# Kernel optimization log

Measured on AMD Instinct MI355X. Metric: run time of the kernel, lower is better.

## Reference

```python
import jax, jax.numpy as jnp
import numpy as np

TEMP = 0.07
POS_WINDOW = 2
EPS = 1e-8
NEG = -1e9  # finite large-negative for masking (safe under vjp)


def _l2norm(x):
    # matches F.normalize(dim=-1) with eps=1e-12
    n = jnp.sqrt(jnp.sum(x * x, axis=-1, keepdims=True))
    return x / jnp.maximum(n, 1e-12)


def setup_inputs() -> dict:
    key = jax.random.key(0)
    k1, k2, k3, k4, k5 = jax.random.split(key, 5)
    B, T, D = 32, 1024, 256
    eeg_enc = jax.random.normal(k1, (B, T, D), dtype=jnp.float32)
    eye_enc = jax.random.normal(k2, (B, T, D), dtype=jnp.float32)
    mask = jax.random.randint(k3, (B, T), 0, 2, dtype=jnp.int32)
    W_eeg = jax.random.normal(k4, (D, D), dtype=jnp.float32) / np.sqrt(D)
    W_eye = jax.random.normal(k5, (D, D), dtype=jnp.float32) / np.sqrt(D)
    return {"eeg_enc": eeg_enc, "eye_enc": eye_enc, "mask": mask,
            "W_eeg": W_eeg, "W_eye": W_eye}


def reference(eeg_enc, eye_enc, mask, W_eeg, W_eye):
    B, T, D = eeg_enc.shape
    valid = mask > 0  # (B,T)
    # nn.Linear(bias=False): x @ W.T, then L2-normalize
    e = _l2norm(jnp.einsum('btd,ed->bte', eeg_enc, W_eeg))
    v = _l2norm(jnp.einsum('btd,ed->bte', eye_enc, W_eye))
    sims = jnp.einsum('bid,bjd->bij', e, v) / TEMP  # (B,T,T)
    # rank of each valid step within the compressed (gathered) ordering
    rank = jnp.cumsum(valid.astype(jnp.int32), axis=-1) - 1  # (B,T)
    band = jnp.abs(rank[:, :, None] - rank[:, None, :]) <= POS_WINDOW
    pair = valid[:, :, None] & valid[:, None, :]  # both steps valid
    pos = pair & band
    # per-row max over positive (banded) entries
    pos_scores = jnp.max(jnp.where(pos, sims, NEG), axis=-1)  # (B,T)
    # logsumexp over valid columns (the gathered sims row)
    lse = jax.nn.logsumexp(jnp.where(valid[:, None, :], sims, NEG), axis=-1)
    row_loss = -(pos_scores - lse)  # (B,T)
    Tv = jnp.sum(valid, axis=-1)  # (B,)
    per_b = jnp.sum(jnp.where(valid, row_loss, 0.0), axis=-1) / jnp.maximum(Tv, 1)
    per_b = jnp.where(Tv >= 2, per_b, 0.0)  # skip samples with <2 valid steps
    return jnp.sum(per_b) / (B + EPS)
```

## Files before the change

### kernel.cpp

```cpp
#include <hip/hip_runtime.h>
#include <hip/hip_bf16.h>

typedef __attribute__((ext_vector_type(8))) short bf16x8;
typedef __attribute__((ext_vector_type(4))) float f32x4;

#define INVT (1.0f/0.07f)

static __device__ __forceinline__ short f2bf(float f){
    unsigned int u = __float_as_uint(f);
    unsigned int r = (u + 0x7fffu + ((u >> 16) & 1u)) >> 16;
    return (short)r;
}
static __device__ __forceinline__ float bf2f(short s){
    return __uint_as_float(((unsigned int)(unsigned short)s) << 16);
}

static __device__ __forceinline__ void gld16(const void* g, void* l){
    __builtin_amdgcn_global_load_lds(
        (const __attribute__((address_space(1))) unsigned int*)g,
        (__attribute__((address_space(3))) unsigned int*)l, 16, 0, 0);
}

__global__ __launch_bounds__(256) void prep_kernel(const float* __restrict__ Weeg,
                                                   const float* __restrict__ Weye,
                                                   const int* __restrict__ mask,
                                                   short* __restrict__ Wout,
                                                   int* __restrict__ rank,
                                                   int* __restrict__ idx,
                                                   int* __restrict__ Tv,
                                                   float* __restrict__ cb,
                                                   float* __restrict__ bsum){
    __shared__ int ssum[256];
    int tid = threadIdx.x;
    if (blockIdx.x < 512){
        int i = blockIdx.x * 256 + tid;
        float v = (i < 65536) ? Weeg[i] : Weye[i - 65536];
        Wout[i] = f2bf(v);
        return;
    }
    int b = blockIdx.x - 512;
    if (tid == 0) bsum[b] = 0.f;
    int local[4]; int s = 0;
    #pragma unroll
    for (int q = 0; q < 4; ++q){
        int t = tid*4 + q;
        local[q] = (mask[b*1024 + t] > 0) ? 1 : 0;
        s += local[q];
    }
    ssum[tid] = s;
    __syncthreads();
    for (int off = 1; off < 256; off <<= 1){
        int add = (tid >= off) ? ssum[tid - off] : 0;
        __syncthreads();
        ssum[tid] += add;
        __syncthreads();
    }
    int run = ssum[tid] - s;
    #pragma unroll
    for (int q = 0; q < 4; ++q){
        int t = tid*4 + q;
        int g = b*1024 + t;
        run += local[q];
        rank[g] = run - 1;
        cb[g]   = local[q] ? 0.0f : -1e9f;
        if (local[q]) idx[b*1024 + run - 1] = t;
    }
    if (tid == 255) Tv[b] = ssum[255];
}

__global__ __launch_bounds__(256, 5) void proj_kernel(const float* __restrict__ Aeeg,
                                                      const float* __restrict__ Aeye,
                                                      const short* __restrict__ Wbf,
                                                      short* __restrict__ Eout,
                                                      short* __restrict__ Vout){
    __shared__ short sW[64 * 256];
    int sel = blockIdx.y;
    const float* A   = sel ? Aeye : Aeeg;
    const short* W   = Wbf + sel * 65536;
    short*       Out = sel ? Vout : Eout;

    int tid = threadIdx.x;
    int w = tid >> 6, lane = tid & 63;
    int l15 = lane & 15, lq = lane >> 4;
    int kb  = lq * 8;
    int row0 = blockIdx.x * 64;

    bf16x8 xf[8];
    {
        const float* ap = A + (size_t)(row0 + w*16 + l15) * 256 + kb;
        #pragma unroll
        for (int g = 0; g < 8; ++g){
            float4 x0 = *(const float4*)(ap + g*32);
            float4 x1 = *(const float4*)(ap + g*32 + 4);
            bf16x8 t;
            t[0]=f2bf(x0.x); t[1]=f2bf(x0.y); t[2]=f2bf(x0.z); t[3]=f2bf(x0.w);
            t[4]=f2bf(x1.x); t[5]=f2bf(x1.y); t[6]=f2bf(x1.z); t[7]=f2bf(x1.w);
            xf[g] = t;
        }
    }

    f32x4 acc[16];
    #pragma unroll
    for (int q = 0; q < 16; ++q) acc[q] = (f32x4){0.f,0.f,0.f,0.f};

    int ro   = lane >> 5;
    int cb_s = lane & 31;
    int s7   = l15 & 7;

    #pragma unroll
    for (int pass = 0; pass < 4; ++pass){
        if (pass) __syncthreads();
        #pragma unroll
        for (int p = 0; p < 8; ++p){
            int rl  = w*16 + p*2 + ro;
            int cbg = cb_s ^ ((p*2 + ro) & 7);
            gld16(W + (size_t)(pass*64 + rl)*256 + cbg*8,
                  &sW[(w*16 + p*2) * 256]);
        }
        __syncthreads();
        #pragma unroll
        for (int nt = 0; nt < 4; ++nt){
            f32x4 c = acc[pass*4 + nt];
            int rbase = (nt*16 + l15) * 256;
            #pragma unroll
            for (int g = 0; g < 8; ++g){
                bf16x8 wf = *(const bf16x8*)&sW[rbase + (((g*4 + lq) ^ s7) << 3)];
                c = __builtin_amdgcn_mfma_f32_16x16x32_bf16(wf, xf[g], c, 0, 0, 0);
            }
            acc[pass*4 + nt] = c;
        }
    }

    float ss = 0.f;
    #pragma unroll
    for (int q = 0; q < 16; ++q){
        #pragma unroll
        for (int r = 0; r < 4; ++r){ float x = acc[q][r]; ss += x*x; }
    }
    ss += __shfl_xor(ss, 16);
    ss += __shfl_xor(ss, 32);
    float scale = 1.0f / fmaxf(sqrtf(ss), 1e-12f);

    short* op = Out + (size_t)(row0 + w*16 + l15) * 256 + lq*4;
    #pragma unroll
    for (int q = 0; q < 16; ++q){
        short4 pk;
        pk.x = f2bf(acc[q][0] * scale);
        pk.y = f2bf(acc[q][1] * scale);
        pk.z = f2bf(acc[q][2] * scale);
        pk.w = f2bf(acc[q][3] * scale);
        *(short4*)(op + ((q >> 2) * 64 + (q & 3) * 16)) = pk;
    }
}

__global__ __launch_bounds__(256, 2) void loss_kernel(const short* __restrict__ E,
                                                      const short* __restrict__ V,
                                                      const float* __restrict__ cb,
                                                      float* __restrict__ psum){
    __shared__ short sV[2][64 * 256];
    __shared__ float sRed[4][32];

    int n  = blockIdx.x;
    int m  = n >> 3;
    int b  = ((m >> 6) << 3) | (n & 7);
    int lm = m & 63;
    int i0 = (lm >> 3) * 128;
    int jb = lm & 7;
    int j0 = jb * 128;

    int tid = threadIdx.x;
    int w = tid >> 6, lane = tid & 63;
    int l15 = lane & 15, lq = lane >> 4;
    int kb = lq * 8;
    int s7 = l15 & 7;

    int ro = lane >> 5;
    int cs = lane & 31;
    const short* Vrow = V + ((size_t)b*1024 + j0 + w*16 + ro) * 256;
    #pragma unroll
    for (int p = 0; p < 8; ++p){
        int rr = (p*2 + ro) & 7;
        gld16(Vrow + (size_t)(p*2)*256 + (size_t)((cs ^ rr) * 8),
              &sV[0][(w*16 + p*2) * 256]);
    }

    bf16x8 af[2][8];
    {
        const short* ep = E + ((size_t)b*1024 + i0 + w*32 + l15) * 256 + kb;
        #pragma unroll
        for (int g = 0; g < 8; ++g){
            af[0][g] = *(const bf16x8*)(ep + g*32);
            af[1][g] = *(const bf16x8*)(ep + 16*256 + g*32);
        }
    }

    float cbv[8];
    #pragma unroll
    for (int ct = 0; ct < 8; ++ct)
        cbv[ct] = cb[b*1024 + j0 + ct*16 + l15];

    f32x4 acc[2][8];
    #pragma unroll
    for (int s = 0; s < 2; ++s)
        #pragma unroll
        for (int ct = 0; ct < 8; ++ct) acc[s][ct] = (f32x4){0.f,0.f,0.f,0.f};

    __syncthreads();

    #pragma unroll
    for (int p = 0; p < 8; ++p){
        int rr = (p*2 + ro) & 7;
        gld16(Vrow + (size_t)(64 + p*2)*256 + (size_t)((cs ^ rr) * 8),
              &sV[1][(w*16 + p*2) * 256]);
    }

    #pragma unroll
    for (int jt = 0; jt < 4; ++jt){
        bf16x8 bf[8];
        #pragma unroll
        for (int g = 0; g < 8; ++g)
            bf[g] = *(const bf16x8*)&sV[0][(jt*16 + l15)*256 + (((g*4 + lq) ^ s7) << 3)];
        #pragma unroll
        for (int g = 0; g < 8; ++g){
            acc[0][jt] = __builtin_amdgcn_mfma_f32_16x16x32_bf16(af[0][g], bf[g], acc[0][jt], 0, 0, 0);
            acc[1][jt] = __builtin_amdgcn_mfma_f32_16x16x32_bf16(af[1][g], bf[g], acc[1][jt], 0, 0, 0);
        }
    }

    __syncthreads();

    #pragma unroll
    for (int jt = 0; jt < 4; ++jt){
        bf16x8 bf[8];
        #pragma unroll
        for (int g = 0; g < 8; ++g)
            bf[g] = *(const bf16x8*)&sV[1][(jt*16 + l15)*256 + (((g*4 + lq) ^ s7) << 3)];
        #pragma unroll
        for (int g = 0; g < 8; ++g){
            acc[0][4+jt] = __builtin_amdgcn_mfma_f32_16x16x32_bf16(af[0][g], bf[g], acc[0][4+jt], 0, 0, 0);
            acc[1][4+jt] = __builtin_amdgcn_mfma_f32_16x16x32_bf16(af[1][g], bf[g], acc[1][4+jt], 0, 0, 0);
        }
    }

    float ls[2][4];
    #pragma unroll
    for (int s = 0; s < 2; ++s){
        #pragma unroll
        for (int r = 0; r < 4; ++r){
            float acv = 0.f;
            #pragma unroll
            for (int ct = 0; ct < 8; ++ct)
                acv += __expf(fmaf(acc[s][ct][r], INVT, cbv[ct]));
            #pragma unroll
            for (int mm = 1; mm < 16; mm <<= 1)
                acv += __shfl_xor(acv, mm);
            ls[s][r] = acv;
        }
    }
    if (l15 == 0){
        #pragma unroll
        for (int s = 0; s < 2; ++s)
            #pragma unroll
            for (int r = 0; r < 4; ++r)
                sRed[w][s*16 + lq*4 + r] = ls[s][r];
    }
    float* pp = psum + (((size_t)(b*8 + jb)) << 10);
    if (lane < 32) pp[i0 + w*32 + lane] = sRed[w][lane];
}

__global__ __launch_bounds__(256) void pos_kernel(const short* __restrict__ E,
                                                  const short* __restrict__ V,
                                                  const int* __restrict__ mask,
                                                  const int* __restrict__ rank,
                                                  const int* __restrict__ idx,
                                                  const int* __restrict__ Tv,
                                                  float* __restrict__ pmax){
    int tid = threadIdx.x;
    int gl  = tid & 15;
    int rf  = (blockIdx.x * 256 + tid) >> 4;
    int b   = rf >> 10;
    if (mask[rf] <= 0) return;

    int ri = rank[rf];
    int tv = Tv[b];
    int lo = ri - 2; if (lo < 0) lo = 0;
    int hi = ri + 2; if (hi > tv - 1) hi = tv - 1;

    const short* epp = E + (size_t)rf * 256 + gl * 16;
    float ev[16];
    {
        bf16x8 e0 = *(const bf16x8*)epp;
        bf16x8 e1 = *(const bf16x8*)(epp + 8);
        #pragma unroll
        for (int k = 0; k < 8; ++k){ ev[k] = bf2f(e0[k]); ev[8+k] = bf2f(e1[k]); }
    }
    float pm = -1e30f;
    for (int r = lo; r <= hi; ++r){
        int j = idx[b*1024 + r];
        const short* vpp = V + ((size_t)(b*1024) + j) * 256 + gl * 16;
        bf16x8 v0 = *(const bf16x8*)vpp;
        bf16x8 v1 = *(const bf16x8*)(vpp + 8);
        float s = 0.f;
        #pragma unroll
        for (int k = 0; k < 8; ++k){
            s = fmaf(ev[k],   bf2f(v0[k]), s);
            s = fmaf(ev[8+k], bf2f(v1[k]), s);
        }
        s += __shfl_xor(s, 1);
        s += __shfl_xor(s, 2);
        s += __shfl_xor(s, 4);
        s += __shfl_xor(s, 8);
        pm = fmaxf(pm, s);
    }
    if (gl == 0) pmax[rf] = pm * INVT;
}

__global__ __launch_bounds__(256) void reduce_kernel(const float* __restrict__ psum,
                                                     const float* __restrict__ pmax,
                                                     const int* __restrict__ mask,
                                                     float* __restrict__ bsum){
    int b  = blockIdx.x >> 2;
    int i  = (blockIdx.x & 3) * 256 + threadIdx.x;
    int g  = b*1024 + i;
    float a = 0.f;
    if (mask[g] > 0){
        const float* pp = psum + ((size_t)b << 13);
        float ps = 0.f;
        #pragma unroll
        for (int s = 0; s < 8; ++s) ps += pp[i + (s << 10)];
        a = logf(ps) - pmax[g];
    }
    #pragma unroll
    for (int m = 1; m < 64; m <<= 1) a += __shfl_xor(a, m);
    if ((threadIdx.x & 63) == 0 && a != 0.f) atomicAdd(&bsum[b], a);
}

__global__ void final_kernel(const float* __restrict__ bsum,
                             const int* __restrict__ Tv,
                             float* __restrict__ out){
    int tid = threadIdx.x;
    float v = 0.f;
    if (tid < 32){
        int tv = Tv[tid];
        if (tv >= 2) v = bsum[tid] / (float)tv;
    }
    #pragma unroll
    for (int m = 1; m < 64; m <<= 1) v += __shfl_xor(v, m);
    if (tid == 0) out[0] = v / 32.0f;
}

extern "C" void kernel_launch(void* const* d_in, const int* in_sizes, int n_in,
                              void* d_out, int out_size, void* d_ws, size_t ws_size,
                              hipStream_t stream) {
    const float* eeg  = (const float*)d_in[0];
    const float* eye  = (const float*)d_in[1];
    const int*   mask = (const int*)d_in[2];
    const float* Weeg = (const float*)d_in[3];
    const float* Weye = (const float*)d_in[4];
    float* out = (float*)d_out;

    char* ws = (char*)d_ws;
    short* e_bf  = (short*)(ws);
    short* v_bf  = (short*)(ws + 16777216);
    short* wbf   = (short*)(ws + 33554432);
    int*   rank  = (int*)  (ws + 33816576);
    int*   idx   = (int*)  (ws + 33947648);
    float* cb    = (float*)(ws + 34078720);
    float* psum  = (float*)(ws + 34209792);
    float* pmax  = (float*)(ws + 35258368);
    int*   Tv    = (int*)  (ws + 35389440);
    float* bsum  = (float*)(ws + 35389568);

    prep_kernel<<<544, 256, 0, stream>>>(Weeg, Weye, mask, wbf, rank, idx, Tv, cb, bsum);
    proj_kernel<<<dim3(512, 2), 256, 0, stream>>>(eeg, eye, wbf, e_bf, v_bf);
    loss_kernel<<<2048, 256, 0, stream>>>(e_bf, v_bf, cb, psum);
    pos_kernel<<<2048, 256, 0, stream>>>(e_bf, v_bf, mask, rank, idx, Tv, pmax);
    reduce_kernel<<<128, 256, 0, stream>>>(psum, pmax, mask, bsum);
    final_kernel<<<1, 64, 0, stream>>>(bsum, Tv, out);
}
```

Measured before the change: 171.0 us.

## Double-buffer W tiles in projection kernel and stage output through LDS

The projection kernel now uses two LDS buffers for W slices. The first two slices are prefetched before the activation load, and each next slice is loaded while the current one feeds the MFMAs, which hides the global-to-LDS latency per pass. The bf16 output is also written into LDS first and then stored to global memory as contiguous 16-byte rows instead of scattered 8-byte stores. LDS use doubles and the occupancy hint drops from 5 to 2 blocks per CU, which may reduce latency hiding across waves.

```diff
diff --git a/kernel.cpp b/kernel.cpp
--- a/kernel.cpp
+++ b/kernel.cpp
@@ -68,12 +68,12 @@
     if (tid == 255) Tv[b] = ssum[255];
 }
 
-__global__ __launch_bounds__(256, 5) void proj_kernel(const float* __restrict__ Aeeg,
+__global__ __launch_bounds__(256, 2) void proj_kernel(const float* __restrict__ Aeeg,
                                                       const float* __restrict__ Aeye,
                                                       const short* __restrict__ Wbf,
                                                       short* __restrict__ Eout,
                                                       short* __restrict__ Vout){
-    __shared__ short sW[64 * 256];
+    __shared__ short sW[2][64 * 256];
     int sel = blockIdx.y;
     const float* A   = sel ? Aeye : Aeeg;
     const short* W   = Wbf + sel * 65536;
@@ -84,6 +84,23 @@
     int l15 = lane & 15, lq = lane >> 4;
     int kb  = lq * 8;
     int row0 = blockIdx.x * 64;
+
+    int ro   = lane >> 5;
+    int cs   = lane & 31;
+    int s7   = l15 & 7;
+
+    #pragma unroll
+    for (int p = 0; p < 8; ++p){
+        int rr = (p*2 + ro) & 7;
+        gld16(W + (size_t)(w*16 + p*2 + ro)*256 + (cs ^ rr)*8,
+              &sW[0][(w*16 + p*2) * 256]);
+    }
+    #pragma unroll
+    for (int p = 0; p < 8; ++p){
+        int rr = (p*2 + ro) & 7;
+        gld16(W + (size_t)(64 + w*16 + p*2 + ro)*256 + (cs ^ rr)*8,
+              &sW[1][(w*16 + p*2) * 256]);
+    }
 
     bf16x8 xf[8];
     {
@@ -103,32 +120,72 @@
     #pragma unroll
     for (int q = 0; q < 16; ++q) acc[q] = (f32x4){0.f,0.f,0.f,0.f};
 
-    int ro   = lane >> 5;
-    int cb_s = lane & 31;
-    int s7   = l15 & 7;
-
-    #pragma unroll
-    for (int pass = 0; pass < 4; ++pass){
-        if (pass) __syncthreads();
-        #pragma unroll
-        for (int p = 0; p < 8; ++p){
-            int rl  = w*16 + p*2 + ro;
-            int cbg = cb_s ^ ((p*2 + ro) & 7);
-            gld16(W + (size_t)(pass*64 + rl)*256 + cbg*8,
-                  &sW[(w*16 + p*2) * 256]);
-        }
-        __syncthreads();
-        #pragma unroll
-        for (int nt = 0; nt < 4; ++nt){
-            f32x4 c = acc[pass*4 + nt];
-            int rbase = (nt*16 + l15) * 256;
-            #pragma unroll
-            for (int g = 0; g < 8; ++g){
-                bf16x8 wf = *(const bf16x8*)&sW[rbase + (((g*4 + lq) ^ s7) << 3)];
-                c = __builtin_amdgcn_mfma_f32_16x16x32_bf16(wf, xf[g], c, 0, 0, 0);
-            }
-            acc[pass*4 + nt] = c;
-        }
+    __syncthreads();
+
+    #pragma unroll
+    for (int nt = 0; nt < 4; ++nt){
+        f32x4 c = acc[nt];
+        int rbase = (nt*16 + l15) * 256;
+        #pragma unroll
+        for (int g = 0; g < 8; ++g){
+            bf16x8 wf = *(const bf16x8*)&sW[0][rbase + (((g*4 + lq) ^ s7) << 3)];
+            c = __builtin_amdgcn_mfma_f32_16x16x32_bf16(wf, xf[g], c, 0, 0, 0);
+        }
+        acc[nt] = c;
+    }
+
+    __syncthreads();
+
+    #pragma unroll
+    for (int p = 0; p < 8; ++p){
+        int rr = (p*2 + ro) & 7;
+        gld16(W + (size_t)(128 + w*16 + p*2 + ro)*256 + (cs ^ rr)*8,
+              &sW[0][(w*16 + p*2) * 256]);
+    }
+    #pragma unroll
+    for (int nt = 0; nt < 4; ++nt){
+        f32x4 c = acc[4 + nt];
+        int rbase = (nt*16 + l15) * 256;
+        #pragma unroll
+        for (int g = 0; g < 8; ++g){
+            bf16x8 wf = *(const bf16x8*)&sW[1][rbase + (((g*4 + lq) ^ s7) << 3)];
+            c = __builtin_amdgcn_mfma_f32_16x16x32_bf16(wf, xf[g], c, 0, 0, 0);
+        }
+        acc[4 + nt] = c;
+    }
+
+    __syncthreads();
+
+    #pragma unroll
+    for (int p = 0; p < 8; ++p){
+        int rr = (p*2 + ro) & 7;
+        gld16(W + (size_t)(192 + w*16 + p*2 + ro)*256 + (cs ^ rr)*8,
+              &sW[1][(w*16 + p*2) * 256]);
+    }
+    #pragma unroll
+    for (int nt = 0; nt < 4; ++nt){
+        f32x4 c = acc[8 + nt];
+        int rbase = (nt*16 + l15) * 256;
+        #pragma unroll
+        for (int g = 0; g < 8; ++g){
+            bf16x8 wf = *(const bf16x8*)&sW[0][rbase + (((g*4 + lq) ^ s7) << 3)];
+            c = __builtin_amdgcn_mfma_f32_16x16x32_bf16(wf, xf[g], c, 0, 0, 0);
+        }
+        acc[8 + nt] = c;
+    }
+
+    __syncthreads();
+
+    #pragma unroll
+    for (int nt = 0; nt < 4; ++nt){
+        f32x4 c = acc[12 + nt];
+        int rbase = (nt*16 + l15) * 256;
+        #pragma unroll
+        for (int g = 0; g < 8; ++g){
+            bf16x8 wf = *(const bf16x8*)&sW[1][rbase + (((g*4 + lq) ^ s7) << 3)];
+            c = __builtin_amdgcn_mfma_f32_16x16x32_bf16(wf, xf[g], c, 0, 0, 0);
+        }
+        acc[12 + nt] = c;
     }
 
     float ss = 0.f;
@@ -141,7 +198,7 @@
     ss += __shfl_xor(ss, 32);
     float scale = 1.0f / fmaxf(sqrtf(ss), 1e-12f);
 
-    short* op = Out + (size_t)(row0 + w*16 + l15) * 256 + lq*4;
+    short* tw = &sW[0][(w*16 + l15) * 256 + lq*4];
     #pragma unroll
     for (int q = 0; q < 16; ++q){
         short4 pk;
@@ -149,7 +206,14 @@
         pk.y = f2bf(acc[q][1] * scale);
         pk.z = f2bf(acc[q][2] * scale);
         pk.w = f2bf(acc[q][3] * scale);
-        *(short4*)(op + ((q >> 2) * 64 + (q & 3) * 16)) = pk;
+        *(short4*)(tw + ((q >> 2) * 64 + (q & 3) * 16)) = pk;
+    }
+    const short* tr = &sW[0][(w*16) * 256];
+    short* op = Out + (size_t)(row0 + w*16) * 256;
+    #pragma unroll
+    for (int p = 0; p < 8; ++p){
+        int s = p*512 + lane*8;
+        *(int4*)(op + s) = *(const int4*)(tr + s);
     }
 }
 
```

After: 168.9 us. Within noise of the previous version (-1.2%).

## Double-buffer weight/V tiles and stage proj output via LDS for coalesced stores

Applied to the files above, without the earlier changes.

The projection kernel now streams the weight matrix in 32-row chunks through a double-buffered LDS ring, so the next chunk's async load overlaps the current MFMAs. Its output is first written to LDS and then stored to global memory as coalesced 16-byte rows. The loss kernel now covers 256 columns per block over 8 pipelined 32-column stages and folds exp-sum into each stage, which cuts accumulator registers and halves block count and partial-sum traffic. The trade-offs are more barriers and a change in occupancy hints.

```diff
diff --git a/kernel.cpp b/kernel.cpp
--- a/kernel.cpp
+++ b/kernel.cpp
@@ -68,12 +68,12 @@
     if (tid == 255) Tv[b] = ssum[255];
 }
 
-__global__ __launch_bounds__(256, 5) void proj_kernel(const float* __restrict__ Aeeg,
+__global__ __launch_bounds__(256, 4) void proj_kernel(const float* __restrict__ Aeeg,
                                                       const float* __restrict__ Aeye,
                                                       const short* __restrict__ Wbf,
                                                       short* __restrict__ Eout,
                                                       short* __restrict__ Vout){
-    __shared__ short sW[64 * 256];
+    __shared__ short sW[2][32 * 256];
     int sel = blockIdx.y;
     const float* A   = sel ? Aeye : Aeeg;
     const short* W   = Wbf + sel * 65536;
@@ -84,6 +84,21 @@
     int l15 = lane & 15, lq = lane >> 4;
     int kb  = lq * 8;
     int row0 = blockIdx.x * 64;
+
+    int ro   = lane >> 5;
+    int cs   = lane & 31;
+    int s7   = l15 & 7;
+
+    #define PROJ_STAGE(ck, buf)                                              \
+        _Pragma("unroll")                                                    \
+        for (int p = 0; p < 4; ++p){                                         \
+            int rr = (p*2 + ro) & 7;                                         \
+            gld16(W + (size_t)((ck)*32 + w*8 + p*2 + ro)*256 + (cs ^ rr)*8,  \
+                  &sW[buf][(w*8 + p*2) * 256]);                              \
+        }
+
+    PROJ_STAGE(0, 0)
+    PROJ_STAGE(1, 1)
 
     bf16x8 xf[8];
     {
@@ -103,33 +118,37 @@
     #pragma unroll
     for (int q = 0; q < 16; ++q) acc[q] = (f32x4){0.f,0.f,0.f,0.f};
 
-    int ro   = lane >> 5;
-    int cb_s = lane & 31;
-    int s7   = l15 & 7;
-
-    #pragma unroll
-    for (int pass = 0; pass < 4; ++pass){
-        if (pass) __syncthreads();
-        #pragma unroll
-        for (int p = 0; p < 8; ++p){
-            int rl  = w*16 + p*2 + ro;
-            int cbg = cb_s ^ ((p*2 + ro) & 7);
-            gld16(W + (size_t)(pass*64 + rl)*256 + cbg*8,
-                  &sW[(w*16 + p*2) * 256]);
-        }
+    __syncthreads();
+
+    #pragma unroll
+    for (int nt = 0; nt < 2; ++nt){
+        f32x4 c = acc[nt];
+        int rbase = (nt*16 + l15) * 256;
+        #pragma unroll
+        for (int g = 0; g < 8; ++g){
+            bf16x8 wf = *(const bf16x8*)&sW[0][rbase + (((g*4 + lq) ^ s7) << 3)];
+            c = __builtin_amdgcn_mfma_f32_16x16x32_bf16(wf, xf[g], c, 0, 0, 0);
+        }
+        acc[nt] = c;
+    }
+
+    #pragma unroll
+    for (int k = 1; k < 8; ++k){
         __syncthreads();
-        #pragma unroll
-        for (int nt = 0; nt < 4; ++nt){
-            f32x4 c = acc[pass*4 + nt];
+        if (k < 7){ PROJ_STAGE(k+1, (k+1)&1) }
+        #pragma unroll
+        for (int nt = 0; nt < 2; ++nt){
+            f32x4 c = acc[k*2 + nt];
             int rbase = (nt*16 + l15) * 256;
             #pragma unroll
             for (int g = 0; g < 8; ++g){
-                bf16x8 wf = *(const bf16x8*)&sW[rbase + (((g*4 + lq) ^ s7) << 3)];
+                bf16x8 wf = *(const bf16x8*)&sW[k&1][rbase + (((g*4 + lq) ^ s7) << 3)];
                 c = __builtin_amdgcn_mfma_f32_16x16x32_bf16(wf, xf[g], c, 0, 0, 0);
             }
-            acc[pass*4 + nt] = c;
-        }
-    }
+            acc[k*2 + nt] = c;
+        }
+    }
+    #undef PROJ_STAGE
 
     float ss = 0.f;
     #pragma unroll
@@ -141,48 +160,67 @@
     ss += __shfl_xor(ss, 32);
     float scale = 1.0f / fmaxf(sqrtf(ss), 1e-12f);
 
-    short* op = Out + (size_t)(row0 + w*16 + l15) * 256 + lq*4;
-    #pragma unroll
-    for (int q = 0; q < 16; ++q){
-        short4 pk;
-        pk.x = f2bf(acc[q][0] * scale);
-        pk.y = f2bf(acc[q][1] * scale);
-        pk.z = f2bf(acc[q][2] * scale);
-        pk.w = f2bf(acc[q][3] * scale);
-        *(short4*)(op + ((q >> 2) * 64 + (q & 3) * 16)) = pk;
-    }
-}
-
-__global__ __launch_bounds__(256, 2) void loss_kernel(const short* __restrict__ E,
+    {
+        int rsel = l15 >> 3;
+        int rloc = w*8 + (l15 & 7);
+        short* twrow = &sW[rsel][rloc * 256];
+        #pragma unroll
+        for (int q = 0; q < 16; ++q){
+            short4 pk;
+            pk.x = f2bf(acc[q][0] * scale);
+            pk.y = f2bf(acc[q][1] * scale);
+            pk.z = f2bf(acc[q][2] * scale);
+            pk.w = f2bf(acc[q][3] * scale);
+            int c   = (q >> 2) * 64 + (q & 3) * 16 + lq*4;
+            int blk = (c >> 3) ^ s7;
+            *(short4*)(twrow + blk*8 + (c & 7)) = pk;
+        }
+        short* op = Out + (size_t)(row0 + w*16) * 256;
+        #pragma unroll
+        for (int p = 0; p < 8; ++p){
+            int r    = p*2 + (lane >> 5);
+            int gblk = lane & 31;
+            const short* tr = &sW[r >> 3][(w*8 + (r & 7)) * 256 + ((gblk ^ (r & 7)) * 8)];
+            *(int4*)(op + r*256 + gblk*8) = *(const int4*)tr;
+        }
+    }
+}
+
+__global__ __launch_bounds__(256, 4) void loss_kernel(const short* __restrict__ E,
                                                       const short* __restrict__ V,
                                                       const float* __restrict__ cb,
                                                       float* __restrict__ psum){
-    __shared__ short sV[2][64 * 256];
+    __shared__ short sV[2][32 * 256];
     __shared__ float sRed[4][32];
 
     int n  = blockIdx.x;
     int m  = n >> 3;
-    int b  = ((m >> 6) << 3) | (n & 7);
-    int lm = m & 63;
-    int i0 = (lm >> 3) * 128;
-    int jb = lm & 7;
-    int j0 = jb * 128;
+    int b  = ((m >> 5) << 3) | (n & 7);
+    int lm = m & 31;
+    int i0 = (lm >> 2) * 128;
+    int js = lm & 3;
+    int j0 = js * 256;
 
     int tid = threadIdx.x;
     int w = tid >> 6, lane = tid & 63;
     int l15 = lane & 15, lq = lane >> 4;
     int kb = lq * 8;
     int s7 = l15 & 7;
-
     int ro = lane >> 5;
     int cs = lane & 31;
-    const short* Vrow = V + ((size_t)b*1024 + j0 + w*16 + ro) * 256;
-    #pragma unroll
-    for (int p = 0; p < 8; ++p){
-        int rr = (p*2 + ro) & 7;
-        gld16(Vrow + (size_t)(p*2)*256 + (size_t)((cs ^ rr) * 8),
-              &sV[0][(w*16 + p*2) * 256]);
-    }
+
+    const short* Vbase = V + ((size_t)b*1024 + j0) * 256;
+
+    #define LOSS_STAGE(ck, buf)                                                   \
+        _Pragma("unroll")                                                         \
+        for (int p = 0; p < 4; ++p){                                              \
+            int rr = (p*2 + ro) & 7;                                              \
+            gld16(Vbase + (size_t)((ck)*32 + w*8 + p*2 + ro)*256 + (cs ^ rr)*8,   \
+                  &sV[buf][(w*8 + p*2) * 256]);                                   \
+        }
+
+    LOSS_STAGE(0, 0)
+    LOSS_STAGE(1, 1)
 
     bf16x8 af[2][8];
     {
@@ -194,67 +232,58 @@
         }
     }
 
-    float cbv[8];
-    #pragma unroll
-    for (int ct = 0; ct < 8; ++ct)
+    float cbv[16];
+    #pragma unroll
+    for (int ct = 0; ct < 16; ++ct)
         cbv[ct] = cb[b*1024 + j0 + ct*16 + l15];
 
-    f32x4 acc[2][8];
-    #pragma unroll
-    for (int s = 0; s < 2; ++s)
-        #pragma unroll
-        for (int ct = 0; ct < 8; ++ct) acc[s][ct] = (f32x4){0.f,0.f,0.f,0.f};
+    float ls[2][4] = {{0.f,0.f,0.f,0.f},{0.f,0.f,0.f,0.f}};
 
     __syncthreads();
 
     #pragma unroll
-    for (int p = 0; p < 8; ++p){
-        int rr = (p*2 + ro) & 7;
-        gld16(Vrow + (size_t)(64 + p*2)*256 + (size_t)((cs ^ rr) * 8),
-              &sV[1][(w*16 + p*2) * 256]);
-    }
-
-    #pragma unroll
-    for (int jt = 0; jt < 4; ++jt){
-        bf16x8 bf[8];
-        #pragma unroll
-        for (int g = 0; g < 8; ++g)
-            bf[g] = *(const bf16x8*)&sV[0][(jt*16 + l15)*256 + (((g*4 + lq) ^ s7) << 3)];
-        #pragma unroll
-        for (int g = 0; g < 8; ++g){
-            acc[0][jt] = __builtin_amdgcn_mfma_f32_16x16x32_bf16(af[0][g], bf[g], acc[0][jt], 0, 0, 0);
-            acc[1][jt] = __builtin_amdgcn_mfma_f32_16x16x32_bf16(af[1][g], bf[g], acc[1][jt], 0, 0, 0);
-        }
-    }
-
-    __syncthreads();
-
-    #pragma unroll
-    for (int jt = 0; jt < 4; ++jt){
-        bf16x8 bf[8];
-        #pragma unroll
-        for (int g = 0; g < 8; ++g)
-            bf[g] = *(const bf16x8*)&sV[1][(jt*16 + l15)*256 + (((g*4 + lq) ^ s7) << 3)];
-        #pragma unroll
-        for (int g = 0; g < 8; ++g){
-            acc[0][4+jt] = __builtin_amdgcn_mfma_f32_16x16x32_bf16(af[0][g], bf[g], acc[0][4+jt], 0, 0, 0);
-            acc[1][4+jt] = __builtin_amdgcn_mfma_f32_16x16x32_bf16(af[1][g], bf[g], acc[1][4+jt], 0, 0, 0);
-        }
-    }
-
-    float ls[2][4];
+    for (int k = 0; k < 8; ++k){
+        if (k > 0) __syncthreads();
+        if (k >= 1 && k < 7){ LOSS_STAGE(k+1, (k+1)&1) }
+        f32x4 acc[2][2];
+        #pragma unroll
+        for (int s = 0; s < 2; ++s)
+            #pragma unroll
+            for (int jt = 0; jt < 2; ++jt) acc[s][jt] = (f32x4){0.f,0.f,0.f,0.f};
+        #pragma unroll
+        for (int jt = 0; jt < 2; ++jt){
+            bf16x8 bfr[8];
+            #pragma unroll
+            for (int g = 0; g < 8; ++g)
+                bfr[g] = *(const bf16x8*)&sV[k&1][(jt*16 + l15)*256 + (((g*4 + lq) ^ s7) << 3)];
+            #pragma unroll
+            for (int g = 0; g < 8; ++g){
+                acc[0][jt] = __builtin_amdgcn_mfma_f32_16x16x32_bf16(af[0][g], bfr[g], acc[0][jt], 0, 0, 0);
+                acc[1][jt] = __builtin_amdgcn_mfma_f32_16x16x32_bf16(af[1][g], bfr[g], acc[1][jt], 0, 0, 0);
+            }
+        }
+        #pragma unroll
+        for (int s = 0; s < 2; ++s){
+            #pragma unroll
+            for (int jt = 0; jt < 2; ++jt){
+                float cbj = cbv[k*2 + jt];
+                #pragma unroll
+                for (int r = 0; r < 4; ++r)
+                    ls[s][r] += __expf(fmaf(acc[s][jt][r], INVT, cbj));
+            }
+        }
+    }
+    #undef LOSS_STAGE
+
     #pragma unroll
     for (int s = 0; s < 2; ++s){
         #pragma unroll
         for (int r = 0; r < 4; ++r){
-            float acv = 0.f;
-            #pragma unroll
-            for (int ct = 0; ct < 8; ++ct)
-                acv += __expf(fmaf(acc[s][ct][r], INVT, cbv[ct]));
+            float v = ls[s][r];
             #pragma unroll
             for (int mm = 1; mm < 16; mm <<= 1)
-                acv += __shfl_xor(acv, mm);
-            ls[s][r] = acv;
+                v += __shfl_xor(v, mm);
+            ls[s][r] = v;
         }
     }
     if (l15 == 0){
@@ -264,7 +293,7 @@
             for (int r = 0; r < 4; ++r)
                 sRed[w][s*16 + lq*4 + r] = ls[s][r];
     }
-    float* pp = psum + (((size_t)(b*8 + jb)) << 10);
+    float* pp = psum + (((size_t)(b*4 + js)) << 10);
     if (lane < 32) pp[i0 + w*32 + lane] = sRed[w][lane];
 }
 
@@ -324,10 +353,8 @@
     int g  = b*1024 + i;
     float a = 0.f;
     if (mask[g] > 0){
-        const float* pp = psum + ((size_t)b << 13);
-        float ps = 0.f;
-        #pragma unroll
-        for (int s = 0; s < 8; ++s) ps += pp[i + (s << 10)];
+        const float* pp = psum + ((size_t)b << 12);
+        float ps = pp[i] + pp[i + 1024] + pp[i + 2048] + pp[i + 3072];
         a = logf(ps) - pmax[g];
     }
     #pragma unroll
@@ -367,13 +394,13 @@
     int*   idx   = (int*)  (ws + 33947648);
     float* cb    = (float*)(ws + 34078720);
     float* psum  = (float*)(ws + 34209792);
-    float* pmax  = (float*)(ws + 35258368);
-    int*   Tv    = (int*)  (ws + 35389440);
-    float* bsum  = (float*)(ws + 35389568);
+    float* pmax  = (float*)(ws + 34734080);
+    int*   Tv    = (int*)  (ws + 34865152);
+    float* bsum  = (float*)(ws + 34865280);
 
     prep_kernel<<<544, 256, 0, stream>>>(Weeg, Weye, mask, wbf, rank, idx, Tv, cb, bsum);
     proj_kernel<<<dim3(512, 2), 256, 0, stream>>>(eeg, eye, wbf, e_bf, v_bf);
-    loss_kernel<<<2048, 256, 0, stream>>>(e_bf, v_bf, cb, psum);
+    loss_kernel<<<1024, 256, 0, stream>>>(e_bf, v_bf, cb, psum);
     pos_kernel<<<2048, 256, 0, stream>>>(e_bf, v_bf, mask, rank, idx, Tv, pmax);
     reduce_kernel<<<128, 256, 0, stream>>>(psum, pmax, mask, bsum);
     final_kernel<<<1, 64, 0, stream>>>(bsum, Tv, out);
```

New measurement: 233.1 us. +36.3%, slower.
